# Optimization experiments

Measured on AMD Instinct MI355X. Metric: run time of the kernel, lower is better.

The kernel has to match this reference:

```python
import jax, jax.numpy as jnp
import numpy as np
from jax import lax

D_MODEL = 1024
D_STATE = 16
D_CONV = 4
EXPAND = 2
DT_RANK = 64
D_INNER = EXPAND * D_MODEL  # 2048
B, L = 2, 2048
LN_EPS = 1e-5


def setup_inputs() -> dict:
    key = jax.random.key(0)
    ks = jax.random.split(key, 8)

    def n(k, shape, s=0.02):
        return jax.random.normal(k, shape, jnp.float32) * s

    # dt_proj bias initialized like mamba_ssm: inverse-softplus of dt in [1e-3, 1e-1]
    dt = jnp.exp(jax.random.uniform(ks[5], (D_INNER,), jnp.float32)
                 * (np.log(0.1) - np.log(0.001)) + np.log(0.001))
    dt_bias = dt + jnp.log(-jnp.expm1(-dt))
    # A_log init: log(1..d_state) per channel (S4D-real init)
    A_init = jnp.tile(jnp.arange(1, D_STATE + 1, dtype=jnp.float32), (D_INNER, 1))

    return {
        "x": jax.random.normal(ks[0], (B, L, D_MODEL), jnp.float32),
        "ln_w": jnp.ones((D_MODEL,), jnp.float32),
        "ln_b": jnp.zeros((D_MODEL,), jnp.float32),
        "in_proj_w": n(ks[1], (2 * D_INNER, D_MODEL)),
        "conv_w": n(ks[2], (D_INNER, D_CONV), 0.1),
        "conv_b": jnp.zeros((D_INNER,), jnp.float32),
        "x_proj_w": n(ks[3], (DT_RANK + 2 * D_STATE, D_INNER)),
        "dt_proj_w": n(ks[4], (D_INNER, DT_RANK), 0.1),
        "dt_proj_b": dt_bias,
        "A_log": jnp.log(A_init),
        "D": jnp.ones((D_INNER,), jnp.float32),
        "out_proj_w": n(ks[6], (D_MODEL, D_INNER)),
    }


def reference(x, ln_w, ln_b, in_proj_w, conv_w, conv_b, x_proj_w,
              dt_proj_w, dt_proj_b, A_log, D, out_proj_w):
    b = x.shape[0]
    # --- pre-norm (LayerNorm) ---
    mu = x.mean(-1, keepdims=True)
    var = jnp.mean(jnp.square(x - mu), axis=-1, keepdims=True)
    xn = (x - mu) * lax.rsqrt(var + LN_EPS) * ln_w + ln_b

    # --- in_proj -> (u, z) ---
    xz = jnp.einsum('bld,ed->ble', xn, in_proj_w)  # (B,L,2*D_INNER)
    u, z = jnp.split(xz, 2, axis=-1)

    # --- causal depthwise conv1d + SiLU ---
    uc = jnp.transpose(u, (0, 2, 1))  # (B, D_INNER, L)
    uc = lax.conv_general_dilated(
        uc, conv_w[:, None, :], window_strides=(1,),
        padding=[(D_CONV - 1, 0)],
        dimension_numbers=('NCH', 'OIH', 'NCH'),
        feature_group_count=D_INNER)
    u = jax.nn.silu(jnp.transpose(uc, (0, 2, 1)) + conv_b)  # (B,L,D_INNER)

    # --- input-dependent dt, B, C ---
    x_dbl = jnp.einsum('bld,ed->ble', u, x_proj_w)  # (B,L,DT_RANK+2*D_STATE)
    dt, Bm, Cm = jnp.split(x_dbl, [DT_RANK, DT_RANK + D_STATE], axis=-1)
    delta = jax.nn.softplus(jnp.einsum('blr,dr->bld', dt, dt_proj_w) + dt_proj_b)

    # --- selective scan ---
    A = -jnp.exp(A_log)  # (D_INNER, D_STATE)
    dA = jnp.exp(jnp.einsum('bld,dn->bldn', delta, A))          # (B,L,D,N)
    dBu = jnp.einsum('bld,bln,bld->bldn', delta, Bm, u)         # (B,L,D,N)

    def step(h, inputs):
        a_t, b_t, c_t = inputs          # (B,D,N), (B,D,N), (B,N)
        h = a_t * h + b_t
        y_t = jnp.einsum('bdn,bn->bd', h, c_t)
        return h, y_t

    h0 = jnp.zeros((b, D_INNER, D_STATE), x.dtype)
    _, ys = lax.scan(step, h0, (dA.transpose(1, 0, 2, 3),
                                dBu.transpose(1, 0, 2, 3),
                                Cm.transpose(1, 0, 2)))  # ys: (L,B,D_INNER)
    y = ys.transpose(1, 0, 2) + u * D  # skip connection via D

    # --- gate + out_proj + residual ---
    y = y * jax.nn.silu(z)
    out = jnp.einsum('bld,ed->ble', y, out_proj_w)
    return out + x
```

## Files before the change

### kernel.cpp

```cpp
#include <hip/hip_runtime.h>
#include <hip/hip_bf16.h>
#include <cstddef>

#define D_MODEL 1024
#define D_STATE 16
#define D_CONV 4
#define DT_RANK 64
#define D_INNER 2048
#define BB 2
#define LL 2048
#define TT (BB * LL)
#define NSEG 64
#define SEGLEN (LL / NSEG)
#define NCHAN (BB * D_INNER)

typedef __bf16 bf16x8 __attribute__((ext_vector_type(8)));
typedef float floatx4 __attribute__((ext_vector_type(4)));
typedef unsigned short ushortx8 __attribute__((ext_vector_type(8)));

__device__ __forceinline__ unsigned short f2bf(float f) {
  unsigned u = __float_as_uint(f);
  unsigned r = u + 0x7FFF + ((u >> 16) & 1);
  return (unsigned short)(r >> 16);
}
__device__ __forceinline__ float b2f(unsigned short v) {
  return __uint_as_float((unsigned)v << 16);
}

__global__ __launch_bounds__(256) void prep_kernel(
    const float* __restrict__ x, const float* __restrict__ lnw,
    const float* __restrict__ lnb, unsigned short* __restrict__ xnb,
    const float* __restrict__ w0, const float* __restrict__ w1,
    const float* __restrict__ w2, const float* __restrict__ w3,
    unsigned short* __restrict__ wdst, float* __restrict__ xd) {
  const int tid = threadIdx.x;
  if (blockIdx.x < TT) {
    int t = blockIdx.x;
    const float4* xr = reinterpret_cast<const float4*>(x + (size_t)t * D_MODEL);
    float4 xv = xr[tid];
    float s = xv.x + xv.y + xv.z + xv.w;
    float sq = xv.x * xv.x + xv.y * xv.y + xv.z * xv.z + xv.w * xv.w;
    for (int off = 32; off >= 1; off >>= 1) {
      s += __shfl_down(s, off);
      sq += __shfl_down(sq, off);
    }
    __shared__ float red[8];
    int wave = tid >> 6;
    if ((tid & 63) == 0) { red[wave * 2] = s; red[wave * 2 + 1] = sq; }
    __syncthreads();
    if (tid == 0) {
      float S = 0.f, Q = 0.f;
      for (int i = 0; i < 4; ++i) { S += red[2 * i]; Q += red[2 * i + 1]; }
      float mean = S * (1.f / D_MODEL);
      float var = Q * (1.f / D_MODEL) - mean * mean;
      red[0] = mean;
      red[1] = rsqrtf(var + 1e-5f);
    }
    __syncthreads();
    float mean = red[0], inv = red[1];
    float4 wv = reinterpret_cast<const float4*>(lnw)[tid];
    float4 bv = reinterpret_cast<const float4*>(lnb)[tid];
    ushort4 o;
    o.x = f2bf((xv.x - mean) * inv * wv.x + bv.x);
    o.y = f2bf((xv.y - mean) * inv * wv.y + bv.y);
    o.z = f2bf((xv.z - mean) * inv * wv.z + bv.z);
    o.w = f2bf((xv.w - mean) * inv * wv.w + bv.w);
    reinterpret_cast<ushort4*>(xnb + (size_t)t * D_MODEL)[tid] = o;
    return;
  }
  int i = (blockIdx.x - TT) * 256 + tid;
  const float* src;
  int off;
  if (i < 1048576) { src = w0; off = 0; }
  else if (i < 1572864) { src = w1; off = 1048576; }
  else if (i < 1622016) { src = w2; off = 1572864; }
  else if (i < 1654784) { src = w3; off = 1622016; }
  else {
    float4 zz = {0.f, 0.f, 0.f, 0.f};
    reinterpret_cast<float4*>(xd)[i - 1654784] = zz;
    return;
  }
  float4 v = reinterpret_cast<const float4*>(src)[i - off];
  ushort4 o;
  o.x = f2bf(v.x); o.y = f2bf(v.y); o.z = f2bf(v.z); o.w = f2bf(v.w);
  reinterpret_cast<ushort4*>(wdst)[i] = o;
}

template <int WNF, int EPI, bool AF32, typename OT>
__global__ __launch_bounds__(256) void gemm_bf16_kernel(
    const void* __restrict__ Ap, int lda,
    const unsigned short* __restrict__ B, int ldb,
    OT* __restrict__ C, int ldc, int M, int N, int K,
    const float* __restrict__ bias, const float* __restrict__ resid, int ldr,
    unsigned short* __restrict__ C2, int kslice) {
  constexpr int BN = WNF * 32;
  constexpr int BSLOTS = BN * 8;
  constexpr int SMEM_USH = 8192 + BN * 64;
  __shared__ unsigned short sm[SMEM_USH];
  unsigned short* Atile = sm;
  unsigned short* Btile = sm + 8192;

  const int tid = threadIdx.x;
  const int lane = tid & 63;
  const int wv = tid >> 6;
  const int wrow = (wv >> 1) * 64;
  const int wcol = (wv & 1) * (WNF * 16);
  int gx = gridDim.x, gy = gridDim.y;
  int lid = blockIdx.y * gx + blockIdx.x;
  int rpx = gy >> 3;
  int xcd = lid & 7;
  int qq0 = lid >> 3;
  int by = xcd * rpx + (qq0 % rpx);
  int bx = qq0 / rpx;
  const int row0 = by * 128;
  const int col0 = bx * BN;
  const int m = lane & 15;
  const int q = lane >> 4;

  int k0lo = 0, k0hi = K;
  if (kslice > 1) {
    int ks = K / kslice;
    k0lo = blockIdx.z * ks;
    k0hi = k0lo + ks;
  }

  floatx4 acc[4][WNF] = {};

  for (int k0 = k0lo; k0 < k0hi; k0 += 64) {
#pragma unroll
    for (int t = 0; t < 4; ++t) {
      int slot = wv * 256 + t * 64 + lane;
      int row = slot >> 3;
      int kg = (slot & 7) ^ (row & 7);
      if (AF32) {
        const float* ga = (const float*)Ap + (size_t)(row0 + row) * lda + k0 + kg * 8;
        float4 v0 = *reinterpret_cast<const float4*>(ga);
        float4 v1 = *reinterpret_cast<const float4*>(ga + 4);
        ushortx8 pk;
        pk[0] = f2bf(v0.x); pk[1] = f2bf(v0.y); pk[2] = f2bf(v0.z); pk[3] = f2bf(v0.w);
        pk[4] = f2bf(v1.x); pk[5] = f2bf(v1.y); pk[6] = f2bf(v1.z); pk[7] = f2bf(v1.w);
        *reinterpret_cast<ushortx8*>(Atile + slot * 8) = pk;
      } else {
        const unsigned short* ga =
            (const unsigned short*)Ap + (size_t)(row0 + row) * lda + k0 + kg * 8;
        __builtin_amdgcn_global_load_lds(
            (const __attribute__((address_space(1))) void*)ga,
            (__attribute__((address_space(3))) void*)(Atile + slot * 8), 16, 0, 0);
      }
    }
#pragma unroll
    for (int t = 0; t < BSLOTS / 256; ++t) {
      int slot = t * 256 + tid;
      int row = slot >> 3;
      int kg = (slot & 7) ^ (row & 7);
      int rowB = col0 + row;
      if (rowB >= N) rowB = N - 1;
      const unsigned short* gb = B + (size_t)rowB * ldb + k0 + kg * 8;
      __builtin_amdgcn_global_load_lds(
          (const __attribute__((address_space(1))) void*)gb,
          (__attribute__((address_space(3))) void*)(Btile + slot * 8), 16, 0, 0);
    }
    __syncthreads();
#pragma unroll
    for (int s = 0; s < 2; ++s) {
      int xr = ((s * 4 + q) ^ (m & 7)) * 8;
      bf16x8 af[4], bfr[WNF];
#pragma unroll
      for (int i = 0; i < 4; ++i)
        af[i] = *reinterpret_cast<const bf16x8*>(
            Atile + (wrow + i * 16 + m) * 64 + xr);
#pragma unroll
      for (int j = 0; j < WNF; ++j)
        bfr[j] = *reinterpret_cast<const bf16x8*>(
            Btile + (wcol + j * 16 + m) * 64 + xr);
#pragma unroll
      for (int i = 0; i < 4; ++i)
#pragma unroll
        for (int j = 0; j < WNF; ++j)
          acc[i][j] = __builtin_amdgcn_mfma_f32_16x16x32_bf16(
              af[i], bfr[j], acc[i][j], 0, 0, 0);
    }
    __syncthreads();
  }

  if (EPI == 1 || EPI == 4) {
    const bool zhalf = (EPI == 4) && (col0 >= D_INNER);
    unsigned short* Cb;
    int cb;
    if (EPI == 4 && col0 >= D_INNER) { Cb = C2; cb = col0 - D_INNER + wcol; }
    else { Cb = (unsigned short*)C; cb = col0 + wcol; }
    constexpr int LPR = WNF * 2;
    constexpr int RPI = 64 / LPR;
#pragma unroll
    for (int round = 0; round < 2; ++round) {
      unsigned short* st = sm + wv * 2112;
      __syncthreads();
#pragma unroll
      for (int ii = 0; ii < 2; ++ii) {
        int i = round * 2 + ii;
#pragma unroll
        for (int j = 0; j < WNF; ++j)
#pragma unroll
          for (int r = 0; r < 4; ++r) {
            float v = acc[i][j][r];
            if (EPI == 1) {
              float xv = v + bias[col0 + wcol + j * 16 + m];
              v = fmaxf(xv, 0.f) + log1pf(expf(-fabsf(xv)));
            } else if (zhalf) {
              v = v / (1.f + expf(-v));
            }
            st[(ii * 16 + q * 4 + r) * 66 + j * 16 + m] = f2bf(v);
          }
      }
      __syncthreads();
#pragma unroll
      for (int t = 0; t < 32 / RPI; ++t) {
        int r = t * RPI + lane / LPR;
        int co = (lane % LPR) * 8;
        ushortx8 val = *reinterpret_cast<const ushortx8*>(st + r * 66 + co);
        *reinterpret_cast<ushortx8*>(
            Cb + (size_t)(row0 + wrow + round * 32 + r) * ldc + cb + co) = val;
      }
    }
  } else {
#pragma unroll
    for (int j = 0; j < WNF; ++j) {
      int gc = col0 + wcol + j * 16 + m;
      if (gc >= N) continue;
#pragma unroll
      for (int i = 0; i < 4; ++i) {
#pragma unroll
        for (int r = 0; r < 4; ++r) {
          int gr = row0 + wrow + i * 16 + q * 4 + r;
          float v = acc[i][j][r];
          if (EPI == 2) {
            ((float*)C)[(size_t)gr * ldc + gc] = v + resid[(size_t)gr * ldr + gc];
          } else {
            if (kslice > 1)
              atomicAdd(&((float*)C)[(size_t)gr * ldc + gc], v);
            else
              ((float*)C)[(size_t)gr * ldc + gc] = v;
          }
        }
      }
    }
  }
}

__global__ __launch_bounds__(256) void conv_silu_kernel(
    const unsigned short* __restrict__ ub, const float* __restrict__ cw,
    const float* __restrict__ cb, unsigned short* __restrict__ ucb) {
  size_t i8 = ((size_t)blockIdx.x * 256 + threadIdx.x) * 8;
  if (i8 >= (size_t)TT * D_INNER) return;
  int d0 = (int)(i8 & (D_INNER - 1));
  int t = (int)(i8 >> 11);
  int l = t & (LL - 1);
  ushortx8 rows[D_CONV];
#pragma unroll
  for (int k = 0; k < D_CONV; ++k) {
    int ll = l - (D_CONV - 1) + k;
    if (ll >= 0)
      rows[k] = *reinterpret_cast<const ushortx8*>(
          ub + i8 - (size_t)(D_CONV - 1 - k) * D_INNER);
    else
      rows[k] = ushortx8{0, 0, 0, 0, 0, 0, 0, 0};
  }
  ushortx8 o;
#pragma unroll
  for (int j = 0; j < 8; ++j) {
    int d = d0 + j;
    float acc = cb[d];
#pragma unroll
    for (int k = 0; k < D_CONV; ++k)
      acc += b2f(rows[k][j]) * cw[d * D_CONV + k];
    o[j] = f2bf(acc / (1.f + expf(-acc)));
  }
  *reinterpret_cast<ushortx8*>(ucb + i8) = o;
}

__global__ __launch_bounds__(256) void scan_partial_kernel(
    const unsigned short* __restrict__ deltab, const unsigned short* __restrict__ ucb,
    const float* __restrict__ xd, const float* __restrict__ A_log,
    float* __restrict__ aprod_buf, float* __restrict__ hend_buf) {
  __shared__ float Bs[SEGLEN][16];
  const int tid = threadIdx.x;
  const int d = blockIdx.x * 256 + tid;
  const int s = blockIdx.y;
  const int b = blockIdx.z;
  const int chan = b * D_INNER + d;
  const size_t tbase = (size_t)b * LL + (size_t)s * SEGLEN;

  {
    int row = tid >> 3, pair = tid & 7;
    *reinterpret_cast<float2*>(&Bs[row][pair * 2]) =
        *reinterpret_cast<const float2*>(xd + (tbase + row) * 96 + 64 + pair * 2);
  }
  floatx4 Ac[4];
  {
    const floatx4* ar = reinterpret_cast<const floatx4*>(A_log + (size_t)d * D_STATE);
#pragma unroll
    for (int k = 0; k < 4; ++k) {
      floatx4 v = ar[k];
      for (int j = 0; j < 4; ++j) Ac[k][j] = -__expf(v[j]) * 1.4426950408889634f;
    }
  }
  __syncthreads();

  floatx4 h[4] = {};
  float S = 0.f;
  for (int l = 0; l < SEGLEN; ++l) {
    size_t t = tbase + l;
    float dl = b2f(deltab[t * D_INNER + d]);
    float ul = b2f(ucb[t * D_INNER + d]);
    float dlul = dl * ul;
    S += dl;
#pragma unroll
    for (int k = 0; k < 4; ++k) {
      floatx4 bv = *reinterpret_cast<const floatx4*>(&Bs[l][k * 4]);
      floatx4 a;
      for (int j = 0; j < 4; ++j) a[j] = __builtin_amdgcn_exp2f(dl * Ac[k][j]);
      h[k] = a * h[k] + dlul * bv;
    }
  }
  size_t base = ((size_t)s * NCHAN + chan) * D_STATE;
#pragma unroll
  for (int k = 0; k < 4; ++k) {
    floatx4 ap;
    for (int j = 0; j < 4; ++j) ap[j] = __builtin_amdgcn_exp2f(S * Ac[k][j]);
    *reinterpret_cast<floatx4*>(hend_buf + base + k * 4) = h[k];
    *reinterpret_cast<floatx4*>(aprod_buf + base + k * 4) = ap;
  }
}

__global__ __launch_bounds__(256) void scan_combine_kernel(
    float* __restrict__ aprod_buf, const float* __restrict__ hend_buf) {
  int idx = blockIdx.x * 256 + threadIdx.x;
  float H = 0.f;
  for (int s = 0; s < NSEG; ++s) {
    size_t si = (size_t)s * (NCHAN * D_STATE) + idx;
    float a = aprod_buf[si];
    float he = hend_buf[si];
    aprod_buf[si] = H;
    H = he + a * H;
  }
}

__global__ __launch_bounds__(256) void scan_final_kernel(
    const unsigned short* __restrict__ deltab, const unsigned short* __restrict__ ucb,
    const float* __restrict__ xd, const unsigned short* __restrict__ zsb,
    const float* __restrict__ A_log, const float* __restrict__ Dv,
    const float* __restrict__ hstart_buf, unsigned short* __restrict__ yb) {
  __shared__ float BCs[SEGLEN][32];
  const int tid = threadIdx.x;
  const int d = blockIdx.x * 256 + tid;
  const int s = blockIdx.y;
  const int b = blockIdx.z;
  const int chan = b * D_INNER + d;
  const size_t tbase = (size_t)b * LL + (size_t)s * SEGLEN;

  {
    int row = tid >> 3, quad = tid & 7;
    *reinterpret_cast<float4*>(&BCs[row][quad * 4]) =
        *reinterpret_cast<const float4*>(xd + (tbase + row) * 96 + 64 + quad * 4);
  }
  floatx4 Ac[4];
  {
    const floatx4* ar = reinterpret_cast<const floatx4*>(A_log + (size_t)d * D_STATE);
#pragma unroll
    for (int k = 0; k < 4; ++k) {
      floatx4 v = ar[k];
      for (int j = 0; j < 4; ++j) Ac[k][j] = -__expf(v[j]) * 1.4426950408889634f;
    }
  }
  float Dd = Dv[d];
  floatx4 h[4];
  {
    size_t base = ((size_t)s * NCHAN + chan) * D_STATE;
#pragma unroll
    for (int k = 0; k < 4; ++k)
      h[k] = *reinterpret_cast<const floatx4*>(hstart_buf + base + k * 4);
  }
  __syncthreads();

  for (int l = 0; l < SEGLEN; ++l) {
    size_t t = tbase + l;
    float dl = b2f(deltab[t * D_INNER + d]);
    float ul = b2f(ucb[t * D_INNER + d]);
    float dlul = dl * ul;
    floatx4 psum = {};
#pragma unroll
    for (int k = 0; k < 4; ++k) {
      floatx4 bv = *reinterpret_cast<const floatx4*>(&BCs[l][k * 4]);
      floatx4 cv = *reinterpret_cast<const floatx4*>(&BCs[l][16 + k * 4]);
      floatx4 a;
      for (int j = 0; j < 4; ++j) a[j] = __builtin_amdgcn_exp2f(dl * Ac[k][j]);
      h[k] = a * h[k] + dlul * bv;
      psum += h[k] * cv;
    }
    float p = psum[0] + psum[1] + psum[2] + psum[3];
    float zs = b2f(zsb[t * D_INNER + d]);
    yb[t * D_INNER + d] = f2bf((p + ul * Dd) * zs);
  }
}

extern "C" void kernel_launch(void* const* d_in, const int* in_sizes, int n_in,
                              void* d_out, int out_size, void* d_ws, size_t ws_size,
                              hipStream_t stream) {
  const float* x         = (const float*)d_in[0];
  const float* ln_w      = (const float*)d_in[1];
  const float* ln_b      = (const float*)d_in[2];
  const float* in_proj_w = (const float*)d_in[3];
  const float* conv_w    = (const float*)d_in[4];
  const float* conv_b    = (const float*)d_in[5];
  const float* x_proj_w  = (const float*)d_in[6];
  const float* dt_proj_w = (const float*)d_in[7];
  const float* dt_proj_b = (const float*)d_in[8];
  const float* A_log     = (const float*)d_in[9];
  const float* Dvec      = (const float*)d_in[10];
  const float* out_proj_w= (const float*)d_in[11];
  float* out = (float*)d_out;

  unsigned short* wip = (unsigned short*)d_ws;
  unsigned short* wop = wip + 4194304;
  unsigned short* wxp = wop + 2097152;
  unsigned short* wdt = wxp + 196608;
  unsigned short* xnb = wdt + 131072;
  unsigned short* ub  = xnb + (size_t)TT * D_MODEL;
  unsigned short* ucb = ub + (size_t)TT * D_INNER;
  unsigned short* zsb = ucb + (size_t)TT * D_INNER;
  unsigned short* deltab = zsb + (size_t)TT * D_INNER;
  float* xd    = (float*)(deltab + (size_t)TT * D_INNER);
  float* hend  = xd + (size_t)TT * 96;
  float* aprod = hend + (size_t)NSEG * NCHAN * D_STATE;

  prep_kernel<<<TT + 6848, 256, 0, stream>>>(x, ln_w, ln_b, xnb, in_proj_w,
                                             out_proj_w, x_proj_w, dt_proj_w,
                                             wip, xd);

  gemm_bf16_kernel<4, 4, false, unsigned short><<<dim3(32, 32), 256, 0, stream>>>(
      xnb, D_MODEL, wip, D_MODEL, ub, D_INNER, TT, 2 * D_INNER, D_MODEL,
      nullptr, nullptr, 0, zsb, 1);

  conv_silu_kernel<<<(TT * D_INNER) / (256 * 8), 256, 0, stream>>>(
      ub, conv_w, conv_b, ucb);

  gemm_bf16_kernel<2, 0, false, float><<<dim3(2, 32, 4), 256, 0, stream>>>(
      ucb, D_INNER, wxp, D_INNER, xd, 96, TT, 96, D_INNER,
      nullptr, nullptr, 0, nullptr, 4);

  gemm_bf16_kernel<4, 1, true, unsigned short><<<dim3(16, 32), 256, 0, stream>>>(
      xd, 96, wdt, DT_RANK, deltab, D_INNER, TT, D_INNER, DT_RANK,
      dt_proj_b, nullptr, 0, nullptr, 1);

  scan_partial_kernel<<<dim3(D_INNER / 256, NSEG, BB), 256, 0, stream>>>(
      deltab, ucb, xd, A_log, aprod, hend);
  scan_combine_kernel<<<(NCHAN * D_STATE) / 256, 256, 0, stream>>>(aprod, hend);
  scan_final_kernel<<<dim3(D_INNER / 256, NSEG, BB), 256, 0, stream>>>(
      deltab, ucb, xd, zsb, A_log, Dvec, aprod, ucb);

  gemm_bf16_kernel<2, 2, false, float><<<dim3(16, 32), 256, 0, stream>>>(
      ucb, D_INNER, wop, D_INNER, out, D_MODEL, TT, D_MODEL, D_INNER,
      nullptr, x, D_MODEL, nullptr, 1);
}
```

Baseline: 336.9 us.

## Fuse dt_proj GEMM with softplus and partial selective scan into one kernel

Replaces the separate dt_proj GEMM and scan_partial kernels with a single dtscan kernel. Each 128x128 tile computes delta with MFMA, applies bias and softplus, writes delta to global, and runs the partial segment scan on delta kept in shared memory. This saves one launch and one global read of delta. The cost is only 512 blocks of 256 threads, each running two 32-step serial scans per thread, which may lower scan parallelism and occupancy compared with the old 2048-block scan grid. GEMM template parameters are also cleaned up, with the bounds clamp made compile-time.

Measured after the change: 325.6 us. -3.4%, faster.

```diff
diff --git a/kernel.cpp b/kernel.cpp
--- a/kernel.cpp
+++ b/kernel.cpp
@@ -86,9 +86,9 @@
   reinterpret_cast<ushort4*>(wdst)[i] = o;
 }
 
-template <int WNF, int EPI, bool AF32, typename OT>
+template <int WNF, int EPI, bool CLAMP, typename OT>
 __global__ __launch_bounds__(256) void gemm_bf16_kernel(
-    const void* __restrict__ Ap, int lda,
+    const unsigned short* __restrict__ A, int lda,
     const unsigned short* __restrict__ B, int ldb,
     OT* __restrict__ C, int ldc, int M, int N, int K,
     const float* __restrict__ bias, const float* __restrict__ resid, int ldr,
@@ -132,21 +132,10 @@
       int slot = wv * 256 + t * 64 + lane;
       int row = slot >> 3;
       int kg = (slot & 7) ^ (row & 7);
-      if (AF32) {
-        const float* ga = (const float*)Ap + (size_t)(row0 + row) * lda + k0 + kg * 8;
-        float4 v0 = *reinterpret_cast<const float4*>(ga);
-        float4 v1 = *reinterpret_cast<const float4*>(ga + 4);
-        ushortx8 pk;
-        pk[0] = f2bf(v0.x); pk[1] = f2bf(v0.y); pk[2] = f2bf(v0.z); pk[3] = f2bf(v0.w);
-        pk[4] = f2bf(v1.x); pk[5] = f2bf(v1.y); pk[6] = f2bf(v1.z); pk[7] = f2bf(v1.w);
-        *reinterpret_cast<ushortx8*>(Atile + slot * 8) = pk;
-      } else {
-        const unsigned short* ga =
-            (const unsigned short*)Ap + (size_t)(row0 + row) * lda + k0 + kg * 8;
-        __builtin_amdgcn_global_load_lds(
-            (const __attribute__((address_space(1))) void*)ga,
-            (__attribute__((address_space(3))) void*)(Atile + slot * 8), 16, 0, 0);
-      }
+      const unsigned short* ga = A + (size_t)(row0 + row) * lda + k0 + kg * 8;
+      __builtin_amdgcn_global_load_lds(
+          (const __attribute__((address_space(1))) void*)ga,
+          (__attribute__((address_space(3))) void*)(Atile + slot * 8), 16, 0, 0);
     }
 #pragma unroll
     for (int t = 0; t < BSLOTS / 256; ++t) {
@@ -154,7 +143,7 @@
       int row = slot >> 3;
       int kg = (slot & 7) ^ (row & 7);
       int rowB = col0 + row;
-      if (rowB >= N) rowB = N - 1;
+      if (CLAMP && rowB >= N) rowB = N - 1;
       const unsigned short* gb = B + (size_t)rowB * ldb + k0 + kg * 8;
       __builtin_amdgcn_global_load_lds(
           (const __attribute__((address_space(1))) void*)gb,
@@ -183,11 +172,11 @@
     __syncthreads();
   }
 
-  if (EPI == 1 || EPI == 4) {
-    const bool zhalf = (EPI == 4) && (col0 >= D_INNER);
+  if (EPI == 4) {
+    const bool zhalf = (col0 >= D_INNER);
     unsigned short* Cb;
     int cb;
-    if (EPI == 4 && col0 >= D_INNER) { Cb = C2; cb = col0 - D_INNER + wcol; }
+    if (zhalf) { Cb = C2; cb = col0 - D_INNER + wcol; }
     else { Cb = (unsigned short*)C; cb = col0 + wcol; }
     constexpr int LPR = WNF * 2;
     constexpr int RPI = 64 / LPR;
@@ -203,12 +192,7 @@
 #pragma unroll
           for (int r = 0; r < 4; ++r) {
             float v = acc[i][j][r];
-            if (EPI == 1) {
-              float xv = v + bias[col0 + wcol + j * 16 + m];
-              v = fmaxf(xv, 0.f) + log1pf(expf(-fabsf(xv)));
-            } else if (zhalf) {
-              v = v / (1.f + expf(-v));
-            }
+            if (zhalf) v = v / (1.f + expf(-v));
             st[(ii * 16 + q * 4 + r) * 66 + j * 16 + m] = f2bf(v);
           }
       }
@@ -226,7 +210,7 @@
 #pragma unroll
     for (int j = 0; j < WNF; ++j) {
       int gc = col0 + wcol + j * 16 + m;
-      if (gc >= N) continue;
+      if (CLAMP && gc >= N) continue;
 #pragma unroll
       for (int i = 0; i < 4; ++i) {
 #pragma unroll
@@ -247,6 +231,157 @@
   }
 }
 
+__global__ __launch_bounds__(256) void dtscan_kernel(
+    const float* __restrict__ xd, const unsigned short* __restrict__ wdt,
+    const float* __restrict__ dtb, const unsigned short* __restrict__ ucb,
+    const float* __restrict__ A_log, unsigned short* __restrict__ deltab,
+    float* __restrict__ aprod_buf, float* __restrict__ hend_buf) {
+  __shared__ unsigned short sm[20736];
+  unsigned short* Atile = sm;
+  unsigned short* Btile = sm + 8192;
+
+  const int tid = threadIdx.x;
+  const int lane = tid & 63;
+  const int wv = tid >> 6;
+  const int wrow = (wv >> 1) * 64;
+  const int wcol = (wv & 1) * 64;
+  int gx = gridDim.x, gy = gridDim.y;
+  int lid = blockIdx.y * gx + blockIdx.x;
+  int rpx = gy >> 3;
+  int xcd = lid & 7;
+  int qq0 = lid >> 3;
+  int by = xcd * rpx + (qq0 % rpx);
+  int bx = qq0 / rpx;
+  const int row0 = by * 128;
+  const int col0 = bx * 128;
+  const int m = lane & 15;
+  const int q = lane >> 4;
+
+#pragma unroll
+  for (int t = 0; t < 4; ++t) {
+    int slot = wv * 256 + t * 64 + lane;
+    int row = slot >> 3;
+    int kg = (slot & 7) ^ (row & 7);
+    const float* ga = xd + (size_t)(row0 + row) * 96 + kg * 8;
+    float4 v0 = *reinterpret_cast<const float4*>(ga);
+    float4 v1 = *reinterpret_cast<const float4*>(ga + 4);
+    ushortx8 pk;
+    pk[0] = f2bf(v0.x); pk[1] = f2bf(v0.y); pk[2] = f2bf(v0.z); pk[3] = f2bf(v0.w);
+    pk[4] = f2bf(v1.x); pk[5] = f2bf(v1.y); pk[6] = f2bf(v1.z); pk[7] = f2bf(v1.w);
+    *reinterpret_cast<ushortx8*>(Atile + slot * 8) = pk;
+  }
+#pragma unroll
+  for (int t = 0; t < 4; ++t) {
+    int slot = t * 256 + tid;
+    int row = slot >> 3;
+    int kg = (slot & 7) ^ (row & 7);
+    const unsigned short* gb = wdt + (size_t)(col0 + row) * DT_RANK + kg * 8;
+    __builtin_amdgcn_global_load_lds(
+        (const __attribute__((address_space(1))) void*)gb,
+        (__attribute__((address_space(3))) void*)(Btile + slot * 8), 16, 0, 0);
+  }
+  __syncthreads();
+  floatx4 acc[4][4] = {};
+#pragma unroll
+  for (int s = 0; s < 2; ++s) {
+    int xr = ((s * 4 + q) ^ (m & 7)) * 8;
+    bf16x8 af[4], bfr[4];
+#pragma unroll
+    for (int i = 0; i < 4; ++i)
+      af[i] = *reinterpret_cast<const bf16x8*>(Atile + (wrow + i * 16 + m) * 64 + xr);
+#pragma unroll
+    for (int j = 0; j < 4; ++j)
+      bfr[j] = *reinterpret_cast<const bf16x8*>(Btile + (wcol + j * 16 + m) * 64 + xr);
+#pragma unroll
+    for (int i = 0; i < 4; ++i)
+#pragma unroll
+      for (int j = 0; j < 4; ++j)
+        acc[i][j] = __builtin_amdgcn_mfma_f32_16x16x32_bf16(
+            af[i], bfr[j], acc[i][j], 0, 0, 0);
+  }
+  __syncthreads();
+
+  unsigned short* st = sm;
+  float* Bf = (float*)(sm + 16640);
+  float bj[4];
+#pragma unroll
+  for (int j = 0; j < 4; ++j) bj[j] = dtb[col0 + wcol + j * 16 + m];
+#pragma unroll
+  for (int i = 0; i < 4; ++i)
+#pragma unroll
+    for (int j = 0; j < 4; ++j)
+#pragma unroll
+      for (int r = 0; r < 4; ++r) {
+        float xv = acc[i][j][r] + bj[j];
+        float sp = fmaxf(xv, 0.f) + log1pf(expf(-fabsf(xv)));
+        int lrow = wrow + i * 16 + q * 4 + r;
+        int lcol = wcol + j * 16 + m;
+        st[lrow * 130 + lcol] = f2bf(sp);
+      }
+#pragma unroll
+  for (int e = 0; e < 2; ++e) {
+    int f4 = e * 256 + tid;
+    int row = f4 >> 2, part = f4 & 3;
+    float4 v = *reinterpret_cast<const float4*>(
+        xd + (size_t)(row0 + row) * 96 + 64 + part * 4);
+    *reinterpret_cast<float4*>(Bf + row * 16 + part * 4) = v;
+  }
+  __syncthreads();
+
+#pragma unroll
+  for (int e = 0; e < 8; ++e) {
+    int c = e * 256 + tid;
+    int rrow = c >> 4, co = (c & 15) * 8;
+    ushortx8 val = *reinterpret_cast<const ushortx8*>(st + rrow * 130 + co);
+    *reinterpret_cast<ushortx8*>(
+        deltab + (size_t)(row0 + rrow) * D_INNER + col0 + co) = val;
+  }
+
+  const int ch = tid & 127;
+  const int sp = tid >> 7;
+  const int d = col0 + ch;
+  const int b = row0 >> 11;
+  const int chan = b * D_INNER + d;
+  floatx4 Ac[4];
+  {
+    const floatx4* ar = reinterpret_cast<const floatx4*>(A_log + (size_t)d * D_STATE);
+#pragma unroll
+    for (int k = 0; k < 4; ++k) {
+      floatx4 v = ar[k];
+      for (int j = 0; j < 4; ++j) Ac[k][j] = -__expf(v[j]) * 1.4426950408889634f;
+    }
+  }
+#pragma unroll
+  for (int ss = 0; ss < 2; ++ss) {
+    int lbase = sp * 64 + ss * 32;
+    int seg = ((row0 & (LL - 1)) >> 5) + sp * 2 + ss;
+    floatx4 h[4] = {};
+    float S = 0.f;
+    for (int l = 0; l < SEGLEN; ++l) {
+      int lr = lbase + l;
+      float dl = b2f(st[lr * 130 + ch]);
+      float ul = b2f(ucb[(size_t)(row0 + lr) * D_INNER + d]);
+      float dlul = dl * ul;
+      S += dl;
+#pragma unroll
+      for (int k = 0; k < 4; ++k) {
+        floatx4 bv = *reinterpret_cast<const floatx4*>(Bf + lr * 16 + k * 4);
+        floatx4 a;
+        for (int j = 0; j < 4; ++j) a[j] = __builtin_amdgcn_exp2f(dl * Ac[k][j]);
+        h[k] = a * h[k] + dlul * bv;
+      }
+    }
+    size_t base = ((size_t)seg * NCHAN + chan) * D_STATE;
+#pragma unroll
+    for (int k = 0; k < 4; ++k) {
+      floatx4 ap;
+      for (int j = 0; j < 4; ++j) ap[j] = __builtin_amdgcn_exp2f(S * Ac[k][j]);
+      *reinterpret_cast<floatx4*>(hend_buf + base + k * 4) = h[k];
+      *reinterpret_cast<floatx4*>(aprod_buf + base + k * 4) = ap;
+    }
+  }
+}
+
 __global__ __launch_bounds__(256) void conv_silu_kernel(
     const unsigned short* __restrict__ ub, const float* __restrict__ cw,
     const float* __restrict__ cb, unsigned short* __restrict__ ucb) {
@@ -276,60 +411,6 @@
     o[j] = f2bf(acc / (1.f + expf(-acc)));
   }
   *reinterpret_cast<ushortx8*>(ucb + i8) = o;
-}
-
-__global__ __launch_bounds__(256) void scan_partial_kernel(
-    const unsigned short* __restrict__ deltab, const unsigned short* __restrict__ ucb,
-    const float* __restrict__ xd, const float* __restrict__ A_log,
-    float* __restrict__ aprod_buf, float* __restrict__ hend_buf) {
-  __shared__ float Bs[SEGLEN][16];
-  const int tid = threadIdx.x;
-  const int d = blockIdx.x * 256 + tid;
-  const int s = blockIdx.y;
-  const int b = blockIdx.z;
-  const int chan = b * D_INNER + d;
-  const size_t tbase = (size_t)b * LL + (size_t)s * SEGLEN;
-
-  {
-    int row = tid >> 3, pair = tid & 7;
-    *reinterpret_cast<float2*>(&Bs[row][pair * 2]) =
-        *reinterpret_cast<const float2*>(xd + (tbase + row) * 96 + 64 + pair * 2);
-  }
-  floatx4 Ac[4];
-  {
-    const floatx4* ar = reinterpret_cast<const floatx4*>(A_log + (size_t)d * D_STATE);
-#pragma unroll
-    for (int k = 0; k < 4; ++k) {
-      floatx4 v = ar[k];
-      for (int j = 0; j < 4; ++j) Ac[k][j] = -__expf(v[j]) * 1.4426950408889634f;
-    }
-  }
-  __syncthreads();
-
-  floatx4 h[4] = {};
-  float S = 0.f;
-  for (int l = 0; l < SEGLEN; ++l) {
-    size_t t = tbase + l;
-    float dl = b2f(deltab[t * D_INNER + d]);
-    float ul = b2f(ucb[t * D_INNER + d]);
-    float dlul = dl * ul;
-    S += dl;
-#pragma unroll
-    for (int k = 0; k < 4; ++k) {
-      floatx4 bv = *reinterpret_cast<const floatx4*>(&Bs[l][k * 4]);
-      floatx4 a;
-      for (int j = 0; j < 4; ++j) a[j] = __builtin_amdgcn_exp2f(dl * Ac[k][j]);
-      h[k] = a * h[k] + dlul * bv;
-    }
-  }
-  size_t base = ((size_t)s * NCHAN + chan) * D_STATE;
-#pragma unroll
-  for (int k = 0; k < 4; ++k) {
-    floatx4 ap;
-    for (int j = 0; j < 4; ++j) ap[j] = __builtin_amdgcn_exp2f(S * Ac[k][j]);
-    *reinterpret_cast<floatx4*>(hend_buf + base + k * 4) = h[k];
-    *reinterpret_cast<floatx4*>(aprod_buf + base + k * 4) = ap;
-  }
 }
 
 __global__ __launch_bounds__(256) void scan_combine_kernel(
@@ -444,16 +525,13 @@
   conv_silu_kernel<<<(TT * D_INNER) / (256 * 8), 256, 0, stream>>>(
       ub, conv_w, conv_b, ucb);
 
-  gemm_bf16_kernel<2, 0, false, float><<<dim3(2, 32, 4), 256, 0, stream>>>(
+  gemm_bf16_kernel<2, 0, true, float><<<dim3(2, 32, 4), 256, 0, stream>>>(
       ucb, D_INNER, wxp, D_INNER, xd, 96, TT, 96, D_INNER,
       nullptr, nullptr, 0, nullptr, 4);
 
-  gemm_bf16_kernel<4, 1, true, unsigned short><<<dim3(16, 32), 256, 0, stream>>>(
-      xd, 96, wdt, DT_RANK, deltab, D_INNER, TT, D_INNER, DT_RANK,
-      dt_proj_b, nullptr, 0, nullptr, 1);
-
-  scan_partial_kernel<<<dim3(D_INNER / 256, NSEG, BB), 256, 0, stream>>>(
-      deltab, ucb, xd, A_log, aprod, hend);
+  dtscan_kernel<<<dim3(16, 32), 256, 0, stream>>>(
+      xd, wdt, dt_proj_b, ucb, A_log, deltab, aprod, hend);
+
   scan_combine_kernel<<<(NCHAN * D_STATE) / 256, 256, 0, stream>>>(aprod, hend);
   scan_final_kernel<<<dim3(D_INNER / 256, NSEG, BB), 256, 0, stream>>>(
       deltab, ucb, xd, zsb, A_log, Dvec, aprod, ucb);
```
